# Optimization experiments

Measured on AMD Instinct MI355X. Metric: run time of the kernel, lower is better.

Reference implementation:

```python
import jax, jax.numpy as jnp
import numpy as np

B, N, C = 16, 2048, 3           # images, proposals/image, classes (incl. background)
K = 100                         # num_detections kept per class
SCORE_THRESH = 0.05
NMS_THRESH = 0.5
MIN_ANGLE = 10.0                # process_box min width (self.min_angle)
WX, WW = 1.0, 1.0               # box_coder reg_weights
NEG = jnp.float32(-1e9)


def setup_inputs() -> dict:
    key = jax.random.key(0)
    k1, k2, k3, k4 = jax.random.split(key, 4)
    class_logit = jax.random.normal(k1, (B, N, C), jnp.float32)
    box_regression = jax.random.normal(k2, (B, N, 2 * C), jnp.float32) * 0.1
    starts = jax.random.uniform(k3, (B, N), dtype=jnp.float32) * 300.0
    widths = jax.random.uniform(k4, (B, N), dtype=jnp.float32) * 50.0 + 12.0
    proposal = jnp.stack([starts, starts + widths], axis=-1)  # [B,N,2] 1-D intervals
    return {"class_logit": class_logit, "box_regression": box_regression,
            "proposal": proposal, "image_shape": 360}


def _decode(delta, prop):
    w = prop[:, 1] - prop[:, 0]
    ctr = prop[:, 0] + 0.5 * w
    dx = delta[:, 0] / WX
    dw = jnp.minimum(delta[:, 1] / WW, 4.0)  # clamp like torchvision
    pc = dx * w + ctr
    pw = jnp.exp(dw) * w
    return jnp.stack([pc - 0.5 * pw, pc + 0.5 * pw], axis=-1)  # [N,2]


def _iou_1d(a, b):
    inter = jnp.maximum(0.0, jnp.minimum(a[:, None, 1], b[None, :, 1])
                        - jnp.maximum(a[:, None, 0], b[None, :, 0]))
    union = (a[:, None, 1] - a[:, None, 0]) + (b[None, :, 1] - b[None, :, 0]) - inter
    return inter / jnp.maximum(union, 1e-8)  # [Na,Nb]


def _infer_one_class(score, delta, prop, image_shape):
    # score [N], delta [N,2], prop [N,2] -> [K,3] (start, end, score); invalid slots score=NEG
    box = _decode(delta, prop)
    lo = jnp.clip(box[:, 0], 0.0, image_shape)
    hi = jnp.clip(box[:, 1], 0.0, image_shape)
    box = jnp.stack([lo, hi], axis=-1)
    valid = ((hi - lo) >= MIN_ANGLE) & (score >= SCORE_THRESH)
    ms = jnp.where(valid, score, NEG)
    order = jnp.argsort(-ms)
    b = box[order]
    s = ms[order]
    sup = jax.lax.stop_gradient(_iou_1d(b, b)) > NMS_THRESH  # [N,N] bool
    idx = jnp.arange(N)

    def body(keep, i):  # greedy NMS in score order
        kill = sup[i] & keep[i] & (idx > i)
        return keep & ~kill, None

    keep0 = s > 0.5 * NEG
    keep, _ = jax.lax.scan(body, keep0, idx)
    ks = jnp.where(keep, s, NEG)
    top_s, top_i = jax.lax.top_k(ks, K)
    top_b = b[top_i]
    return jnp.concatenate([top_b, top_s[:, None]], axis=-1)  # [K,3]


def reference(class_logit, box_regression, proposal, image_shape):
    img = jnp.float32(image_shape)
    scores = jax.nn.softmax(class_logit, axis=-1)[..., 1:]        # [B,N,C-1] fg classes
    deltas = box_regression.reshape(B, N, C, 2)[:, :, 1:]         # [B,N,C-1,2]
    scores = jnp.moveaxis(scores, -1, 1)                          # [B,C-1,N]
    deltas = jnp.moveaxis(deltas, 2, 1)                           # [B,C-1,N,2]
    f = jax.vmap(jax.vmap(_infer_one_class, in_axes=(0, 0, None, None)),
                 in_axes=(0, 0, 0, None))
    return f(scores, deltas, proposal, img)  # [B, C-1, K, 3]
```

## Files before the change

kernel.cpp:

```cpp
#include <hip/hip_runtime.h>
#include <math.h>

#define B_IMG 16
#define N_PROP 2048
#define C_CLS 3
#define K_OUT 100
#define NTHREADS 1024
#define NWAVES (NTHREADS / 64)
#define NBLK64 (N_PROP / 64)
#define NUNITS (B_IMG * N_PROP)
#define NTHA 256
#define RUN 512

__device__ __forceinline__ unsigned long long shfl_xor_u64(unsigned long long v, int lx) {
    unsigned int lo = (unsigned int)__shfl_xor((int)(unsigned int)(v & 0xffffffffull), lx, 64);
    unsigned int hi = (unsigned int)__shfl_xor((int)(unsigned int)(v >> 32), lx, 64);
    return ((unsigned long long)hi << 32) | (unsigned long long)lo;
}
__device__ __forceinline__ float readlane_f(float v, int l) {
    return __int_as_float(__builtin_amdgcn_readlane(__float_as_int(v), l));
}
__device__ __forceinline__ unsigned long long readlane_u64(unsigned long long v, int l) {
    unsigned int lo = (unsigned int)__builtin_amdgcn_readlane((int)(unsigned int)(v & 0xffffffffull), l);
    unsigned int hi = (unsigned int)__builtin_amdgcn_readlane((int)(unsigned int)(v >> 32), l);
    return ((unsigned long long)hi << 32) | (unsigned long long)lo;
}
__device__ __forceinline__ bool iou_gt_half(float inter, float uni) {
    double b = (double)fmaxf(uni, 1e-8f);
    return (double)inter * 2.0 > b * 0x1.000001p0;
}
__device__ __forceinline__ float parse_imgf(int raw) {
    return (raw > 0 && raw < 1000000) ? (float)raw : __int_as_float(raw);
}

__global__ __launch_bounds__(NTHA)
void decode_sort_kernel(const float* __restrict__ class_logit,
                        const float* __restrict__ box_reg,
                        const float* __restrict__ proposal,
                        const int* __restrict__ image_shape_p,
                        unsigned long long* __restrict__ wskey,
                        float2* __restrict__ wbox)
{
#pragma clang fp contract(off)
    __shared__ unsigned long long skey[RUN];

    const int tid = threadIdx.x;
    const int lane = tid & 63;
    const int wid = tid >> 6;
    const int u = blockIdx.x >> 2;
    const int q = blockIdx.x & 3;
    const int img = u >> 1;
    const int cls = u & 1;
    const bool flip = (q & 1) != 0;
    const int off = q * RUN;
    const size_t base = (size_t)cls * NUNITS + (size_t)img * N_PROP;
    const float imgf = parse_imgf(image_shape_p[0]);

    for (int i = tid; i < RUN; i += NTHA) {
        const int n = off + i;
        const size_t g = (size_t)img * N_PROP + n;
        const float* lg = class_logit + g * C_CLS;
        float l0 = lg[0], l1 = lg[1], l2 = lg[2];
        float mx = fmaxf(l0, fmaxf(l1, l2));
        float e0 = (float)exp((double)(l0 - mx));
        float e1 = (float)exp((double)(l1 - mx));
        float e2 = (float)exp((double)(l2 - mx));
        float denom = (e0 + e1) + e2;
        float score = ((cls == 0) ? e1 : e2) / denom;

        const float* dr = box_reg + g * (2 * C_CLS) + 2 * (cls + 1);
        float dx = dr[0];
        float dw = fminf(dr[1], 4.0f);
        const float* pp = proposal + g * 2;
        float pA = pp[0], pB = pp[1];
        float w = pB - pA;
        float ctr = pA + 0.5f * w;
        float tt = dx * w;
        float pc = tt + ctr;
        float pw = (float)exp((double)dw) * w;
        float half = 0.5f * pw;
        float lo = pc - half;
        float hi = pc + half;
        lo = fminf(fmaxf(lo, 0.0f), imgf);
        hi = fminf(fmaxf(hi, 0.0f), imgf);
        bool valid = ((hi - lo) >= 10.0f) && (score >= 0.05f);
        float ms = valid ? score : -1e9f;
        wbox[base + n] = make_float2(lo, hi);
        unsigned int uu = __float_as_uint(ms);
        unsigned int e = (uu & 0x80000000u) ? ~uu : (uu | 0x80000000u);
        skey[i] = ((unsigned long long)e << 32) |
                  (unsigned long long)(0xFFFFFFFFu - (unsigned int)n);
    }
    __syncthreads();

    const int p0 = (wid << 7) | (lane << 1);
    const int p1 = p0 | 1;
    unsigned long long r0 = skey[p0], r1 = skey[p1];

    auto pass_inreg = [&](int k, int j) {
        bool desc = (((p0 & k) == 0) != flip);
        if (j == 1) {
            bool sw = desc ? (r0 < r1) : (r0 > r1);
            if (sw) { unsigned long long t = r0; r0 = r1; r1 = t; }
        } else {
            int lx = j >> 1;
            unsigned long long o0 = shfl_xor_u64(r0, lx);
            unsigned long long o1 = shfl_xor_u64(r1, lx);
            bool lower = ((p0 & j) == 0);
            bool takeMax = (lower == desc);
            r0 = takeMax ? (r0 > o0 ? r0 : o0) : (r0 < o0 ? r0 : o0);
            r1 = takeMax ? (r1 > o1 ? r1 : o1) : (r1 < o1 ? r1 : o1);
        }
    };

    for (int k = 2; k <= 128; k <<= 1)
        for (int j = k >> 1; j >= 1; j >>= 1)
            pass_inreg(k, j);

    for (int k = 256; k <= RUN; k <<= 1) {
        skey[p0] = r0; skey[p1] = r1;
        __syncthreads();
        for (int j = k >> 1; j >= 128; j >>= 1) {
            int i = ((tid & ~(j - 1)) << 1) | (tid & (j - 1));
            int part = i | j;
            unsigned long long a = skey[i], b = skey[part];
            bool desc_blk = (((i & k) == 0) != flip);
            bool sw = desc_blk ? (a < b) : (a > b);
            if (sw) { skey[i] = b; skey[part] = a; }
            __syncthreads();
        }
        r0 = skey[p0]; r1 = skey[p1];
        for (int j = 64; j >= 1; j >>= 1)
            pass_inreg(k, j);
    }
    wskey[base + off + p0] = r0;
    wskey[base + off + p1] = r1;
}

__global__ __launch_bounds__(NTHREADS)
void roiheads_kernel(const unsigned long long* __restrict__ wskey,
                     const float2* __restrict__ wbox,
                     float* __restrict__ out)
{
#pragma clang fp contract(off)
    __shared__ unsigned long long skey[N_PROP];
    __shared__ float slo[N_PROP], shi[N_PROP];
    __shared__ unsigned char keep[N_PROP];
    __shared__ unsigned short alv[2][N_PROP];
    __shared__ float clo[64], chi[64];
    __shared__ unsigned long long sup[64];
    __shared__ unsigned long long kmask[NBLK64];
    __shared__ int wsum[NWAVES];
    __shared__ int sh_nvalid;

    const int tid = threadIdx.x;
    const int lane = tid & 63;
    const int wid = tid >> 6;
    const int img = blockIdx.x >> 1;
    const int cls = blockIdx.x & 1;
    const size_t base = (size_t)cls * NUNITS + (size_t)img * N_PROP;

    if (tid == 0) sh_nvalid = 0;

    const int p0 = (wid << 7) | (lane << 1);
    const int p1 = p0 | 1;

    unsigned long long r0 = wskey[base + p0];
    unsigned long long r1 = wskey[base + p1];

    auto pass_inreg = [&](int k, int j) {
        if (j == 1) {
            bool desc = ((p0 & k) == 0);
            bool sw = desc ? (r0 < r1) : (r0 > r1);
            if (sw) { unsigned long long t = r0; r0 = r1; r1 = t; }
        } else {
            int lx = j >> 1;
            unsigned long long o0 = shfl_xor_u64(r0, lx);
            unsigned long long o1 = shfl_xor_u64(r1, lx);
            bool desc = ((p0 & k) == 0);
            bool lower = ((p0 & j) == 0);
            bool takeMax = (lower == desc);
            r0 = takeMax ? (r0 > o0 ? r0 : o0) : (r0 < o0 ? r0 : o0);
            r1 = takeMax ? (r1 > o1 ? r1 : o1) : (r1 < o1 ? r1 : o1);
        }
    };

    for (int k = 1024; k <= N_PROP; k <<= 1) {
        skey[p0] = r0; skey[p1] = r1;
        __syncthreads();
        for (int j = k >> 1; j >= 128; j >>= 1) {
            int i = ((tid & ~(j - 1)) << 1) | (tid & (j - 1));
            int part = i | j;
            unsigned long long a = skey[i], b = skey[part];
            bool desc_blk = ((i & k) == 0);
            bool sw = desc_blk ? (a < b) : (a > b);
            if (sw) { skey[i] = b; skey[part] = a; }
            __syncthreads();
        }
        r0 = skey[p0]; r1 = skey[p1];
        for (int j = 64; j >= 1; j >>= 1)
            pass_inreg(k, j);
    }
    skey[p0] = r0; skey[p1] = r1;
    __syncthreads();

    for (int i = tid; i < N_PROP; i += NTHREADS) {
        unsigned long long kk = skey[i];
        unsigned int e = (unsigned int)(kk >> 32);
        unsigned int sb = (e & 0x80000000u) ? (e & 0x7FFFFFFFu) : ~e;
        float s = __uint_as_float(sb);
        unsigned int n = 0xFFFFFFFFu - (unsigned int)(kk & 0xFFFFFFFFull);
        float2 bx = wbox[base + n];
        slo[i] = bx.x;
        shi[i] = bx.y;
        keep[i] = 0;
        bool v = (s > -5e8f);
        unsigned long long mb = __ballot(v);
        if (lane == 0) atomicAdd(&sh_nvalid, __popcll(mb));
        alv[0][i] = (unsigned short)i;
    }
    __syncthreads();

    int na = sh_nvalid;
    int cur = 0;
    int tk = 0;
    const unsigned long long below = (1ull << lane) - 1ull;

    while (na > 0) {
        const int m = (na < 64) ? na : 64;

        unsigned short cp = alv[cur][lane];
        bool cin = (lane < m);
        float qloc = cin ? slo[cp] : 0.0f;
        float qhic = cin ? shi[cp] : 0.0f;

#pragma unroll
        for (int rr4 = 0; rr4 < 4; ++rr4) {
            int rr = (wid << 2) | rr4;
            unsigned long long row = 0;
            if (rr < m) {
                unsigned short rp = alv[cur][rr];
                float rlo = slo[rp], rhi = shi[rp];
                float inter = fmaxf(fminf(rhi, qhic) - fmaxf(rlo, qloc), 0.0f);
                float uni = (rhi - rlo) + (qhic - qloc) - inter;
                bool kill = cin && (lane > rr) && iou_gt_half(inter, uni);
                row = __ballot(kill);
            }
            if (lane == 0) sup[rr] = row;
        }
        __syncthreads();

        unsigned long long rw = sup[lane];
        unsigned long long A = (m >= 64) ? ~0ull : ((1ull << m) - 1ull);
        unsigned long long kept = 0;
        while (A) {
            int c = __builtin_ctzll(A);
            kept |= (1ull << c);
            A &= ~(readlane_u64(rw, c) | (1ull << c));
        }
        const int cnt = __popcll(kept);

        if (wid == 0) {
            bool alive = cin && ((kept >> lane) & 1ull);
            if (alive) {
                keep[cp] = 1;
                int rank = __popcll(kept & below);
                clo[rank] = qloc; chi[rank] = qhic;
            }
        }
        __syncthreads();
        tk += cnt;
        if (tk >= K_OUT) break;

        float klo = 0.0f, khi = 0.0f;
        if (lane < cnt) { klo = clo[lane]; khi = chi[lane]; }
        int base2 = 0;
        for (int start = 64; start < na; start += NTHREADS) {
            int t2 = start + tid;
            unsigned short qq = 0;
            bool surv = false;
            if (t2 < na) {
                qq = alv[cur][t2];
                float qlo = slo[qq], qhi = shi[qq];
                float qw = qhi - qlo;
                bool dead = false;
                for (int r = 0; r < cnt; ++r) {
                    float cl = readlane_f(klo, r);
                    float ch = readlane_f(khi, r);
                    float inter = fmaxf(fminf(qhi, ch) - fmaxf(qlo, cl), 0.0f);
                    float uni = qw + (ch - cl) - inter;
                    dead |= iou_gt_half(inter, uni);
                }
                surv = !dead;
            }
            unsigned long long mb = __ballot(surv);
            if (lane == 0) wsum[wid] = __popcll(mb);
            __syncthreads();
            int off2 = base2, tot = base2;
            for (int w2 = 0; w2 < NWAVES; ++w2) {
                int c2 = wsum[w2];
                if (w2 < wid) off2 += c2;
                tot += c2;
            }
            if (surv) alv[cur ^ 1][off2 + __popcll(mb & below)] = qq;
            base2 = tot;
            __syncthreads();
        }
        na = base2;
        cur ^= 1;
    }

    for (int blk = wid; blk < NBLK64; blk += NWAVES) {
        bool kk = keep[blk * 64 + lane] != 0;
        unsigned long long mb = __ballot(kk);
        if (lane == 0) kmask[blk] = mb;
    }
    __syncthreads();
    {
        float* outp = out + (((size_t)img * 2 + cls) * K_OUT) * 3;
        for (int blk = wid; blk < NBLK64; blk += NWAVES) {
            int kc = 0, nc = 0, nk = 0;
            for (int b = 0; b < NBLK64; ++b) {
                int pc = __popcll(kmask[b]);
                nk += pc;
                if (b < blk) { kc += pc; nc += 64 - pc; }
            }
            if (kc >= K_OUT && nk + nc >= K_OUT && nc >= K_OUT) continue;
            int p = blk * 64 + lane;
            unsigned long long mb = kmask[blk];
            bool k = (mb >> lane) & 1ull;
            int rk = kc + __popcll(mb & below);
            int rn = nc + __popcll((~mb) & below);
            if (k) {
                if (rk < K_OUT) {
                    unsigned long long kk2 = skey[p];
                    unsigned int e = (unsigned int)(kk2 >> 32);
                    unsigned int sb = (e & 0x80000000u) ? (e & 0x7FFFFFFFu) : ~e;
                    outp[rk * 3 + 0] = slo[p];
                    outp[rk * 3 + 1] = shi[p];
                    outp[rk * 3 + 2] = __uint_as_float(sb);
                }
            } else {
                int oi = nk + rn;
                if (oi < K_OUT) {
                    outp[oi * 3 + 0] = slo[p];
                    outp[oi * 3 + 1] = shi[p];
                    outp[oi * 3 + 2] = -1e9f;
                }
            }
        }
    }
}

extern "C" void kernel_launch(void* const* d_in, const int* in_sizes, int n_in,
                              void* d_out, int out_size, void* d_ws, size_t ws_size,
                              hipStream_t stream) {
    const float* class_logit = (const float*)d_in[0];
    const float* box_reg     = (const float*)d_in[1];
    const float* prop        = (const float*)d_in[2];
    const int*   image_shape = (const int*)d_in[3];
    float* out = (float*)d_out;

    unsigned long long* wskey = (unsigned long long*)d_ws;
    float2* wbox = (float2*)((char*)d_ws + 2 * NUNITS * sizeof(unsigned long long));

    decode_sort_kernel<<<dim3(B_IMG * 2 * 4), dim3(NTHA), 0, stream>>>(
        class_logit, box_reg, prop, image_shape, wskey, wbox);
    roiheads_kernel<<<dim3(B_IMG * 2), dim3(NTHREADS), 0, stream>>>(
        wskey, wbox, out);
}
```

Baseline: 95.40 us.

## Fuse decode/partial-sort kernel into NMS kernel, keeping boxes in LDS

After: 97.16 us. No clear change (+1.8%).

```diff
diff --git a/kernel.cpp b/kernel.cpp
--- a/kernel.cpp
+++ b/kernel.cpp
@@ -8,9 +8,6 @@
 #define NTHREADS 1024
 #define NWAVES (NTHREADS / 64)
 #define NBLK64 (N_PROP / 64)
-#define NUNITS (B_IMG * N_PROP)
-#define NTHA 256
-#define RUN 512
 
 __device__ __forceinline__ unsigned long long shfl_xor_u64(unsigned long long v, int lx) {
     unsigned int lo = (unsigned int)__shfl_xor((int)(unsigned int)(v & 0xffffffffull), lx, 64);
@@ -33,31 +30,41 @@
     return (raw > 0 && raw < 1000000) ? (float)raw : __int_as_float(raw);
 }
 
-__global__ __launch_bounds__(NTHA)
-void decode_sort_kernel(const float* __restrict__ class_logit,
-                        const float* __restrict__ box_reg,
-                        const float* __restrict__ proposal,
-                        const int* __restrict__ image_shape_p,
-                        unsigned long long* __restrict__ wskey,
-                        float2* __restrict__ wbox)
+__global__ __launch_bounds__(NTHREADS)
+void roiheads_fused(const float* __restrict__ class_logit,
+                    const float* __restrict__ box_reg,
+                    const float* __restrict__ proposal,
+                    const int* __restrict__ image_shape_p,
+                    float* __restrict__ out)
 {
 #pragma clang fp contract(off)
-    __shared__ unsigned long long skey[RUN];
+    __shared__ unsigned long long skey[N_PROP];
+    __shared__ float blo_n[N_PROP], bhi_n[N_PROP];
+    __shared__ float slo[N_PROP], shi[N_PROP];
+    __shared__ unsigned char keep[N_PROP];
+    __shared__ unsigned short alv[2][N_PROP];
+    __shared__ float clo[64], chi[64];
+    __shared__ unsigned long long sup[64];
+    __shared__ unsigned long long kmask[NBLK64];
+    __shared__ int wsum[NWAVES];
+    __shared__ int sh_nvalid;
 
     const int tid = threadIdx.x;
     const int lane = tid & 63;
     const int wid = tid >> 6;
-    const int u = blockIdx.x >> 2;
-    const int q = blockIdx.x & 3;
-    const int img = u >> 1;
-    const int cls = u & 1;
-    const bool flip = (q & 1) != 0;
-    const int off = q * RUN;
-    const size_t base = (size_t)cls * NUNITS + (size_t)img * N_PROP;
+    const int img = blockIdx.x >> 1;
+    const int cls = blockIdx.x & 1;
     const float imgf = parse_imgf(image_shape_p[0]);
 
-    for (int i = tid; i < RUN; i += NTHA) {
-        const int n = off + i;
+    if (tid == 0) sh_nvalid = 0;
+
+    const int p0 = (wid << 7) | (lane << 1);
+    const int p1 = p0 | 1;
+
+    unsigned long long r0 = 0, r1 = 0;
+#pragma unroll
+    for (int e = 0; e < 2; ++e) {
+        const int n = p0 + e;
         const size_t g = (size_t)img * N_PROP + n;
         const float* lg = class_logit + g * C_CLS;
         float l0 = lg[0], l1 = lg[1], l2 = lg[2];
@@ -85,88 +92,14 @@
         hi = fminf(fmaxf(hi, 0.0f), imgf);
         bool valid = ((hi - lo) >= 10.0f) && (score >= 0.05f);
         float ms = valid ? score : -1e9f;
-        wbox[base + n] = make_float2(lo, hi);
+        blo_n[n] = lo;
+        bhi_n[n] = hi;
         unsigned int uu = __float_as_uint(ms);
-        unsigned int e = (uu & 0x80000000u) ? ~uu : (uu | 0x80000000u);
-        skey[i] = ((unsigned long long)e << 32) |
-                  (unsigned long long)(0xFFFFFFFFu - (unsigned int)n);
-    }
-    __syncthreads();
-
-    const int p0 = (wid << 7) | (lane << 1);
-    const int p1 = p0 | 1;
-    unsigned long long r0 = skey[p0], r1 = skey[p1];
-
-    auto pass_inreg = [&](int k, int j) {
-        bool desc = (((p0 & k) == 0) != flip);
-        if (j == 1) {
-            bool sw = desc ? (r0 < r1) : (r0 > r1);
-            if (sw) { unsigned long long t = r0; r0 = r1; r1 = t; }
-        } else {
-            int lx = j >> 1;
-            unsigned long long o0 = shfl_xor_u64(r0, lx);
-            unsigned long long o1 = shfl_xor_u64(r1, lx);
-            bool lower = ((p0 & j) == 0);
-            bool takeMax = (lower == desc);
-            r0 = takeMax ? (r0 > o0 ? r0 : o0) : (r0 < o0 ? r0 : o0);
-            r1 = takeMax ? (r1 > o1 ? r1 : o1) : (r1 < o1 ? r1 : o1);
-        }
-    };
-
-    for (int k = 2; k <= 128; k <<= 1)
-        for (int j = k >> 1; j >= 1; j >>= 1)
-            pass_inreg(k, j);
-
-    for (int k = 256; k <= RUN; k <<= 1) {
-        skey[p0] = r0; skey[p1] = r1;
-        __syncthreads();
-        for (int j = k >> 1; j >= 128; j >>= 1) {
-            int i = ((tid & ~(j - 1)) << 1) | (tid & (j - 1));
-            int part = i | j;
-            unsigned long long a = skey[i], b = skey[part];
-            bool desc_blk = (((i & k) == 0) != flip);
-            bool sw = desc_blk ? (a < b) : (a > b);
-            if (sw) { skey[i] = b; skey[part] = a; }
-            __syncthreads();
-        }
-        r0 = skey[p0]; r1 = skey[p1];
-        for (int j = 64; j >= 1; j >>= 1)
-            pass_inreg(k, j);
-    }
-    wskey[base + off + p0] = r0;
-    wskey[base + off + p1] = r1;
-}
-
-__global__ __launch_bounds__(NTHREADS)
-void roiheads_kernel(const unsigned long long* __restrict__ wskey,
-                     const float2* __restrict__ wbox,
-                     float* __restrict__ out)
-{
-#pragma clang fp contract(off)
-    __shared__ unsigned long long skey[N_PROP];
-    __shared__ float slo[N_PROP], shi[N_PROP];
-    __shared__ unsigned char keep[N_PROP];
-    __shared__ unsigned short alv[2][N_PROP];
-    __shared__ float clo[64], chi[64];
-    __shared__ unsigned long long sup[64];
-    __shared__ unsigned long long kmask[NBLK64];
-    __shared__ int wsum[NWAVES];
-    __shared__ int sh_nvalid;
-
-    const int tid = threadIdx.x;
-    const int lane = tid & 63;
-    const int wid = tid >> 6;
-    const int img = blockIdx.x >> 1;
-    const int cls = blockIdx.x & 1;
-    const size_t base = (size_t)cls * NUNITS + (size_t)img * N_PROP;
-
-    if (tid == 0) sh_nvalid = 0;
-
-    const int p0 = (wid << 7) | (lane << 1);
-    const int p1 = p0 | 1;
-
-    unsigned long long r0 = wskey[base + p0];
-    unsigned long long r1 = wskey[base + p1];
+        unsigned int enc = (uu & 0x80000000u) ? ~uu : (uu | 0x80000000u);
+        unsigned long long key = ((unsigned long long)enc << 32) |
+                                 (unsigned long long)(0xFFFFFFFFu - (unsigned int)n);
+        if (e == 0) r0 = key; else r1 = key;
+    }
 
     auto pass_inreg = [&](int k, int j) {
         if (j == 1) {
@@ -185,7 +118,11 @@
         }
     };
 
-    for (int k = 1024; k <= N_PROP; k <<= 1) {
+    for (int k = 2; k <= 128; k <<= 1)
+        for (int j = k >> 1; j >= 1; j >>= 1)
+            pass_inreg(k, j);
+
+    for (int k = 256; k <= N_PROP; k <<= 1) {
         skey[p0] = r0; skey[p1] = r1;
         __syncthreads();
         for (int j = k >> 1; j >= 128; j >>= 1) {
@@ -210,9 +147,8 @@
         unsigned int sb = (e & 0x80000000u) ? (e & 0x7FFFFFFFu) : ~e;
         float s = __uint_as_float(sb);
         unsigned int n = 0xFFFFFFFFu - (unsigned int)(kk & 0xFFFFFFFFull);
-        float2 bx = wbox[base + n];
-        slo[i] = bx.x;
-        shi[i] = bx.y;
+        slo[i] = blo_n[n];
+        shi[i] = bhi_n[n];
         keep[i] = 0;
         bool v = (s > -5e8f);
         unsigned long long mb = __ballot(v);
@@ -360,12 +296,8 @@
     const float* prop        = (const float*)d_in[2];
     const int*   image_shape = (const int*)d_in[3];
     float* out = (float*)d_out;
-
-    unsigned long long* wskey = (unsigned long long*)d_ws;
-    float2* wbox = (float2*)((char*)d_ws + 2 * NUNITS * sizeof(unsigned long long));
-
-    decode_sort_kernel<<<dim3(B_IMG * 2 * 4), dim3(NTHA), 0, stream>>>(
-        class_logit, box_reg, prop, image_shape, wskey, wbox);
-    roiheads_kernel<<<dim3(B_IMG * 2), dim3(NTHREADS), 0, stream>>>(
-        wskey, wbox, out);
-}
+    (void)d_ws; (void)ws_size;
+
+    roiheads_fused<<<dim3(B_IMG * 2), dim3(NTHREADS), 0, stream>>>(
+        class_logit, box_reg, prop, image_shape, out);
+}
```
